# Kernel tuning notes

Hardware: AMD Instinct MI355X
Metric: run time of the kernel (lower is better)

Reference implementation:

```python
import jax, jax.numpy as jnp
import numpy as np

B, L, F, P, E, H, D, C, V = 256, 100, 8, 4, 64, 4, 64, 32, 10000
HD = H * D  # 256 = att_dim * head_num
TOWER_IN = F * E + F * E + P * E + C  # 1312
LN_EPS = 1e-3  # keras LayerNormalization default epsilon


def _ln(x, g, b):
    m = jnp.mean(x, axis=-1, keepdims=True)
    v = jnp.mean(jnp.square(x - m), axis=-1, keepdims=True)
    return (x - m) * jax.lax.rsqrt(v + LN_EPS) * g + b


def setup_inputs() -> dict:
    key = jax.random.key(0)
    ks = jax.random.split(key, 32)
    w = lambda k, s: jax.random.normal(k, s, jnp.float32) * 0.02
    inp = {
        'target_ad': jax.random.randint(ks[0], (B, F), 0, V),
        'ubs_feature': jax.random.randint(ks[1], (B, L, F), 0, V),
        'profile_feature': jax.random.randint(ks[2], (B, P), 0, V),
        'context_feature': jax.random.normal(ks[3], (B, C), jnp.float32),
        # embedding tables: one per sparse feature, stacked
        'item_tables': w(ks[4], (F, V, E)),
        'profile_tables': w(ks[5], (P, V, E)),
        # per-timestep distinct attention weights, stacked over L
        'q_w': w(ks[6], (L, E, HD)),
        'k_w': w(ks[7], (L, E, HD)),
        'v_w': w(ks[8], (L, E, HD)),
        'lin_w': w(ks[9], (L, HD, E)),
        'lin_b': jnp.zeros((L, E), jnp.float32),
        # shared post-attention layernorm
        'ln_g': jnp.ones((E,), jnp.float32),
        'ln_b': jnp.zeros((E,), jnp.float32),
        # dense tower
        't_w1': w(ks[10], (TOWER_IN, 1024)), 't_b1': jnp.zeros((1024,), jnp.float32),
        't_g1': jnp.ones((1024,), jnp.float32), 't_bb1': jnp.zeros((1024,), jnp.float32),
        't_w2': w(ks[11], (1024, 512)), 't_b2': jnp.zeros((512,), jnp.float32),
        't_g2': jnp.ones((512,), jnp.float32), 't_bb2': jnp.zeros((512,), jnp.float32),
        't_w3': w(ks[12], (512, 256)), 't_b3': jnp.zeros((256,), jnp.float32),
        't_g3': jnp.ones((256,), jnp.float32), 't_bb3': jnp.zeros((256,), jnp.float32),
        't_w4': w(ks[13], (256, 1)), 't_b4': jnp.zeros((1,), jnp.float32),
    }
    return inp


def reference(target_ad, ubs_feature, profile_feature, context_feature,
              item_tables, profile_tables, q_w, k_w, v_w, lin_w, lin_b,
              ln_g, ln_b,
              t_w1, t_b1, t_g1, t_bb1,
              t_w2, t_b2, t_g2, t_bb2,
              t_w3, t_b3, t_g3, t_bb3,
              t_w4, t_b4):
    b = target_ad.shape[0]
    # embedding lookups (feature-wise tables)
    te = item_tables[jnp.arange(F)[None, :], target_ad]              # [B,F,E]
    ue = item_tables[jnp.arange(F)[None, None, :], ubs_feature]      # [B,L,F,E]
    pe = profile_tables[jnp.arange(P)[None, :], profile_feature]     # [B,P,E]

    # per-step distinct Q/K/V projections, batched over L via einsum
    q = jnp.einsum('blfe,leo->blfo', ue, q_w).reshape(b, L, F, H, D)
    k = jnp.einsum('blfe,leo->blfo', ue, k_w).reshape(b, L, F, H, D)
    v = jnp.einsum('blfe,leo->blfo', ue, v_w).reshape(b, L, F, H, D)
    scores = jnp.einsum('blfhd,blghd->blhfg', q, k) / jnp.sqrt(jnp.float32(D))
    attw = jax.nn.softmax(scores, axis=-1)                           # [B,L,H,F,F]
    att = jnp.einsum('blhfg,blghd->blfhd', attw, v).reshape(b, L, F, HD)
    att_out = jnp.einsum('blfo,loe->blfe', att, lin_w) + lin_b[None, :, None, :]
    # shared LayerNorm per step, summed over L (original accumulates into zeros_like)
    ubs_t = jnp.sum(_ln(att_out, ln_g, ln_b), axis=1)                # [B,F,E]
    ubs = jax.nn.relu(ubs_t / jnp.float32(L))

    total = jnp.concatenate([ubs.reshape(b, -1), te.reshape(b, -1),
                             pe.reshape(b, -1), context_feature], axis=-1)

    h = jax.nn.relu(_ln(total @ t_w1 + t_b1, t_g1, t_bb1))
    h = jax.nn.relu(_ln(h @ t_w2 + t_b2, t_g2, t_bb2))
    h = jax.nn.relu(_ln(h @ t_w3 + t_b3, t_g3, t_bb3))
    out = jax.nn.sigmoid(h @ t_w4 + t_b4)                            # [B,1]
    return out
```

## Files before the change

kernel.cpp:

```cpp
#include <hip/hip_runtime.h>
#include <hip/hip_bf16.h>

#define B_ 256
#define L_ 100
#define F_ 8
#define P_ 4
#define E_ 64
#define H_ 4
#define D_ 64
#define C_ 32
#define V_ 10000
#define TOWER_IN_ 1312
#define LN_EPS 0.001f
#define LCHMAX_ 5
#define NCH_ 24
#define ZK_ 40
#define ATTN_BLKS_ (NCH_ * 32)

typedef __attribute__((ext_vector_type(8))) short bf8v;
typedef __attribute__((ext_vector_type(8))) unsigned short us8;
typedef __attribute__((ext_vector_type(4))) float f4v;

__device__ __forceinline__ unsigned short f2bf(float x) {
    __hip_bfloat16 h = __float2bfloat16(x);
    return __builtin_bit_cast(unsigned short, h);
}

#define BARRIER() do { \
    asm volatile("s_waitcnt lgkmcnt(0)" ::: "memory"); \
    __builtin_amdgcn_s_barrier(); \
    asm volatile("" ::: "memory"); \
} while (0)

__global__ __launch_bounds__(256) void pre_kernel(
    const float* __restrict__ q_w, const float* __restrict__ k_w,
    const float* __restrict__ v_w, const float* __restrict__ lin_w,
    unsigned short* __restrict__ wsMT, unsigned short* __restrict__ wsWT,
    float* __restrict__ ubs_acc)
{
    __shared__ float sA[64][68];
    __shared__ float sB[64][68];
    const int t = threadIdx.x;
    const int bx = blockIdx.x;

    if (bx >= 400) {
        const int bi = bx - 400;
        float4 z = {0.f, 0.f, 0.f, 0.f};
        *(float4*)(ubs_acc + (size_t)bi * 1024 + t * 4) = z;
        return;
    }

    const int l = bx >> 2;
    const int h = bx & 3;
    const size_t obase = (size_t)(l * 4 + h) * 4096;
    const int te = t & 15, to = t >> 4;

    for (int i = 0; i < 16; ++i) {
        int idx = t + i * 256;
        int e = idx >> 6, d = idx & 63;
        sA[e][d] = q_w[(l * 64 + e) * 256 + h * 64 + d];
        sB[e][d] = k_w[(l * 64 + e) * 256 + h * 64 + d];
    }
    __syncthreads();
    {
        float acc[4][4];
        #pragma unroll
        for (int i = 0; i < 4; ++i)
            #pragma unroll
            for (int j = 0; j < 4; ++j) acc[i][j] = 0.f;
        for (int d0 = 0; d0 < 64; d0 += 4) {
            float4 a4[4], b4[4];
            #pragma unroll
            for (int i = 0; i < 4; ++i) a4[i] = *(const float4*)&sA[te + 16 * i][d0];
            #pragma unroll
            for (int j = 0; j < 4; ++j) b4[j] = *(const float4*)&sB[to + 16 * j][d0];
            #pragma unroll
            for (int i = 0; i < 4; ++i)
                #pragma unroll
                for (int j = 0; j < 4; ++j) {
                    acc[i][j] += a4[i].x * b4[j].x;
                    acc[i][j] += a4[i].y * b4[j].y;
                    acc[i][j] += a4[i].z * b4[j].z;
                    acc[i][j] += a4[i].w * b4[j].w;
                }
        }
        #pragma unroll
        for (int j = 0; j < 4; ++j)
            #pragma unroll
            for (int i = 0; i < 4; ++i)
                wsMT[obase + (to + 16 * j) * 64 + (te + 16 * i)] = f2bf(acc[i][j]);
    }
    __syncthreads();

    for (int i = 0; i < 16; ++i) {
        int idx = t + i * 256;
        int e = idx >> 6, d = idx & 63;
        sA[e][d] = v_w[(l * 64 + e) * 256 + h * 64 + d];
        int oo = idx & 63, dd = idx >> 6;
        sB[oo][dd] = lin_w[l * 16384 + (h * 64 + dd) * 64 + oo];
    }
    __syncthreads();
    {
        float acc[4][4];
        #pragma unroll
        for (int i = 0; i < 4; ++i)
            #pragma unroll
            for (int j = 0; j < 4; ++j) acc[i][j] = 0.f;
        for (int d0 = 0; d0 < 64; d0 += 4) {
            float4 a4[4], b4[4];
            #pragma unroll
            for (int i = 0; i < 4; ++i) a4[i] = *(const float4*)&sA[te + 16 * i][d0];
            #pragma unroll
            for (int j = 0; j < 4; ++j) b4[j] = *(const float4*)&sB[to + 16 * j][d0];
            #pragma unroll
            for (int i = 0; i < 4; ++i)
                #pragma unroll
                for (int j = 0; j < 4; ++j) {
                    acc[i][j] += a4[i].x * b4[j].x;
                    acc[i][j] += a4[i].y * b4[j].y;
                    acc[i][j] += a4[i].z * b4[j].z;
                    acc[i][j] += a4[i].w * b4[j].w;
                }
        }
        #pragma unroll
        for (int j = 0; j < 4; ++j)
            #pragma unroll
            for (int i = 0; i < 4; ++i)
                wsWT[obase + (to + 16 * j) * 64 + (te + 16 * i)] = f2bf(acc[i][j]);
    }
}

__global__ __launch_bounds__(256, 3) void attn_kernel(
    const int* __restrict__ ubs_feature, const float* __restrict__ item_tables,
    const unsigned short* __restrict__ wsMT, const unsigned short* __restrict__ wsWT,
    const float* __restrict__ lin_b, const float* __restrict__ ln_g,
    const float* __restrict__ ln_b, float* __restrict__ ubs_acc,
    const float* __restrict__ w1, const float* __restrict__ w2,
    const float* __restrict__ w3,
    unsigned short* __restrict__ Wt1, unsigned short* __restrict__ Wt2,
    unsigned short* __restrict__ Wt3)
{
    __shared__ __align__(16) unsigned short sUE[64][72];
    __shared__ __align__(16) unsigned short sT[64][136];
    __shared__ __align__(16) unsigned short sZt[4][64][ZK_];
    __shared__ __align__(16) unsigned short sAblk[4][16][32];
    __shared__ float sLng[64], sLnb[64], sLinb[LCHMAX_][64];

    const int t = threadIdx.x;

    if (blockIdx.x >= ATTN_BLKS_) {
        float (*tile)[33] = (float (*)[33])sT;
        int bi = blockIdx.x - ATTN_BLKS_;
        const float* src; unsigned short* dst; int K, N, tk, tn;
        if (bi < 1312)      { src = w1; dst = Wt1; K = 1312; N = 1024; tk = bi / 32;  tn = bi % 32; }
        else if (bi < 1824) { int i = bi - 1312; src = w2; dst = Wt2; K = 1024; N = 512; tk = i / 16; tn = i % 16; }
        else                { int i = bi - 1824; src = w3; dst = Wt3; K = 512;  N = 256; tk = i / 8;  tn = i % 8; }
        const int k0 = tk * 32, n0 = tn * 32;
        const int rr = t >> 5, cc = t & 31;
        #pragma unroll
        for (int i = 0; i < 4; ++i) {
            int r = rr * 4 + i;
            tile[r][cc] = src[(size_t)(k0 + r) * N + n0 + cc];
        }
        __syncthreads();
        #pragma unroll
        for (int i = 0; i < 4; ++i) {
            int r = rr * 4 + i;
            dst[(size_t)(n0 + r) * K + k0 + cc] = f2bf(tile[cc][r]);
        }
        return;
    }

    const int c = blockIdx.x >> 5;
    const int lch   = (c < 4) ? 5 : 4;
    const int lbase = (c < 4) ? c * 5 : 20 + (c - 4) * 4;
    const int b0 = (blockIdx.x & 31) * 8;
    const int wv = t >> 6, lane = t & 63, quad = lane >> 4, cl = lane & 15;
    const int role = wv >> 1, hlw = wv & 1;

    const int grow = wv * 16 + (lane >> 2);
    const int gseg = lane & 3;
    const int gb = b0 + (grow >> 3), gf = grow & 7;

    if (t < 64) { sLng[t] = ln_g[t]; sLnb[t] = ln_b[t]; }
    if (t >= 64 && t < 128) {
        for (int li = 0; li < lch; ++li)
            sLinb[li][t - 64] = lin_b[(lbase + li) * 64 + (t - 64)];
    }

    int vidx[LCHMAX_];
    for (int li = 0; li < lch; ++li)
        vidx[li] = ubs_feature[(gb * L_ + lbase + li) * F_ + gf];

    float4 pf[4];
    bf8v bfrag[4][2];

    auto load_bfrag = [&](int lh) {
        const unsigned short* Bsrc = (role == 0 ? wsMT : wsWT) + ((size_t)lh * 4096);
        #pragma unroll
        for (int nt = 0; nt < 4; ++nt)
            #pragma unroll
            for (int k2 = 0; k2 < 2; ++k2)
                bfrag[nt][k2] = *(const bf8v*)(Bsrc + (nt * 16 + cl) * 64 + k2 * 32 + quad * 8);
    };
    auto load_pf = [&](int li) {
        const float* srcp = item_tables + ((size_t)gf * V_ + vidx[li]) * 64 + gseg * 16;
        #pragma unroll
        for (int j = 0; j < 4; ++j) pf[j] = ((const float4*)srcp)[j];
    };
    auto store_ue = [&]() {
        us8 u0, u1;
        u0[0] = f2bf(pf[0].x); u0[1] = f2bf(pf[0].y); u0[2] = f2bf(pf[0].z); u0[3] = f2bf(pf[0].w);
        u0[4] = f2bf(pf[1].x); u0[5] = f2bf(pf[1].y); u0[6] = f2bf(pf[1].z); u0[7] = f2bf(pf[1].w);
        u1[0] = f2bf(pf[2].x); u1[1] = f2bf(pf[2].y); u1[2] = f2bf(pf[2].z); u1[3] = f2bf(pf[2].w);
        u1[4] = f2bf(pf[3].x); u1[5] = f2bf(pf[3].y); u1[6] = f2bf(pf[3].z); u1[7] = f2bf(pf[3].w);
        *(us8*)&sUE[grow][gseg * 16]     = u0;
        *(us8*)&sUE[grow][gseg * 16 + 8] = u1;
    };

    load_pf(0);
    load_bfrag(lbase * 4 + hlw);
    store_ue();
    BARRIER();

    float lnacc[16];
    #pragma unroll
    for (int i = 0; i < 16; ++i) lnacc[i] = 0.f;

    for (int li = 0; li < lch; ++li) {
        const int l = lbase + li;

        if (li + 1 < lch) load_pf(li + 1);

        f4v accO[4];
        #pragma unroll
        for (int nt = 0; nt < 4; ++nt) accO[nt] = {0.f, 0.f, 0.f, 0.f};

        #pragma unroll
        for (int half = 0; half < 2; ++half) {
            #pragma unroll
            for (int m = 0; m < 4; ++m) {
                bf8v a0 = *(const bf8v*)&sUE[m * 16 + cl][quad * 8];
                bf8v a1 = *(const bf8v*)&sUE[m * 16 + cl][32 + quad * 8];
                #pragma unroll
                for (int nt = 0; nt < 4; ++nt) {
                    f4v acc = {0.f, 0.f, 0.f, 0.f};
                    acc = __builtin_amdgcn_mfma_f32_16x16x32_bf16(a0, bfrag[nt][0], acc, 0, 0, 0);
                    acc = __builtin_amdgcn_mfma_f32_16x16x32_bf16(a1, bfrag[nt][1], acc, 0, 0, 0);
                    if (role == 0) {
                        #pragma unroll
                        for (int j = 0; j < 4; ++j)
                            sT[m * 16 + quad * 4 + j][hlw * 64 + nt * 16 + cl] = f2bf(acc[j]);
                    } else {
                        ushort4 zp;
                        zp.x = f2bf(acc[0]); zp.y = f2bf(acc[1]);
                        zp.z = f2bf(acc[2]); zp.w = f2bf(acc[3]);
                        const int k0 = (quad >> 1) * 16 + hlw * 8 + (quad & 1) * 4;
                        *(ushort4*)&sZt[m][nt * 16 + cl][k0] = zp;
                    }
                }
            }
            if (half == 0)          load_bfrag(l * 4 + 2 + hlw);
            else if (li + 1 < lch)  load_bfrag((l + 1) * 4 + hlw);
            BARRIER();

            {
                const int p = wv;
                const bool valid = (cl >> 3) == (quad >> 1);
                bf8v u0 = *(const bf8v*)&sUE[p * 16 + cl][quad * 8];
                bf8v u1 = *(const bf8v*)&sUE[p * 16 + cl][32 + quad * 8];
                #pragma unroll
                for (int hl = 0; hl < 2; ++hl) {
                    bf8v a0s = *(const bf8v*)&sT[p * 16 + cl][hl * 64 + quad * 8];
                    bf8v a1s = *(const bf8v*)&sT[p * 16 + cl][hl * 64 + 32 + quad * 8];
                    f4v acc = {0.f, 0.f, 0.f, 0.f};
                    acc = __builtin_amdgcn_mfma_f32_16x16x32_bf16(a0s, u0, acc, 0, 0, 0);
                    acc = __builtin_amdgcn_mfma_f32_16x16x32_bf16(a1s, u1, acc, 0, 0, 0);
                    const int kk = hl * 8 + (cl & 7) + (cl >> 3) * 16;
                    #pragma unroll
                    for (int j = 0; j < 4; ++j) {
                        float v = acc[j] * 0.125f;
                        float mx = v;
                        mx = fmaxf(mx, __shfl_xor(mx, 1));
                        mx = fmaxf(mx, __shfl_xor(mx, 2));
                        mx = fmaxf(mx, __shfl_xor(mx, 4));
                        float ex = __expf(v - mx);
                        float sm = ex;
                        sm += __shfl_xor(sm, 1);
                        sm += __shfl_xor(sm, 2);
                        sm += __shfl_xor(sm, 4);
                        float aw = valid ? ex * __builtin_amdgcn_rcpf(sm) : 0.f;
                        sAblk[p][quad * 4 + j][kk] = f2bf(aw);
                    }
                }
            }

            {
                const int p = wv;
                bf8v a0p = *(const bf8v*)&sAblk[p][cl][quad * 8];
                #pragma unroll
                for (int nt = 0; nt < 4; ++nt) {
                    bf8v bz = *(const bf8v*)&sZt[p][nt * 16 + cl][quad * 8];
                    accO[nt] = __builtin_amdgcn_mfma_f32_16x16x32_bf16(a0p, bz, accO[nt], 0, 0, 0);
                }
            }
            if (half == 1 && li + 1 < lch) store_ue();
            BARRIER();
        }

        {
            float x[16];
            #pragma unroll
            for (int nt = 0; nt < 4; ++nt)
                #pragma unroll
                for (int j = 0; j < 4; ++j)
                    x[nt * 4 + j] = accO[nt][j] + sLinb[li][nt * 16 + cl];
            #pragma unroll
            for (int j = 0; j < 4; ++j) {
                float s = x[j] + x[4 + j] + x[8 + j] + x[12 + j];
                #pragma unroll
                for (int m = 1; m < 16; m <<= 1) s += __shfl_xor(s, m);
                float mean = s * (1.f / 64.f);
                float q = 0.f;
                #pragma unroll
                for (int nt = 0; nt < 4; ++nt) { float d = x[nt * 4 + j] - mean; q += d * d; }
                #pragma unroll
                for (int m = 1; m < 16; m <<= 1) q += __shfl_xor(q, m);
                float rst = rsqrtf(q * (1.f / 64.f) + LN_EPS);
                #pragma unroll
                for (int nt = 0; nt < 4; ++nt) {
                    int col = nt * 16 + cl;
                    lnacc[nt * 4 + j] += (x[nt * 4 + j] - mean) * rst * sLng[col] + sLnb[col];
                }
            }
        }
    }

    #pragma unroll
    for (int j = 0; j < 4; ++j) {
        const int row = wv * 16 + quad * 4 + j;
        const int b = b0 + (row >> 3), f = row & 7;
        #pragma unroll
        for (int nt = 0; nt < 4; ++nt)
            atomicAdd(&ubs_acc[(size_t)b * 512 + f * 64 + nt * 16 + cl], lnacc[nt * 4 + j]);
    }
}

__device__ __forceinline__ void gemm_from_lds(
    const unsigned short* sA, int lda,
    const unsigned short* __restrict__ Bw, const float* __restrict__ bias,
    float* __restrict__ Cd, int K, int N, int n0w, int m0,
    int quad, int cl)
{
    f4v acc0 = {0.f, 0.f, 0.f, 0.f};
    f4v acc1 = {0.f, 0.f, 0.f, 0.f};
    const unsigned short* arow = sA + cl * lda + quad * 8;
    const unsigned short* brow = Bw + (size_t)(n0w + cl) * K + quad * 8;
    int k0 = 0;
    for (; k0 + 64 <= K; k0 += 64) {
        bf8v a0 = *(const bf8v*)(arow + k0);
        bf8v b0 = *(const bf8v*)(brow + k0);
        bf8v a1 = *(const bf8v*)(arow + k0 + 32);
        bf8v b1 = *(const bf8v*)(brow + k0 + 32);
        acc0 = __builtin_amdgcn_mfma_f32_16x16x32_bf16(a0, b0, acc0, 0, 0, 0);
        acc1 = __builtin_amdgcn_mfma_f32_16x16x32_bf16(a1, b1, acc1, 0, 0, 0);
    }
    if (k0 < K) {
        bf8v a = *(const bf8v*)(arow + k0);
        bf8v b = *(const bf8v*)(brow + k0);
        acc0 = __builtin_amdgcn_mfma_f32_16x16x32_bf16(a, b, acc0, 0, 0, 0);
    }
    float bv = bias[n0w + cl];
    #pragma unroll
    for (int j = 0; j < 4; ++j)
        Cd[(size_t)(m0 + quad * 4 + j) * N + n0w + cl] = acc0[j] + acc1[j] + bv;
}

__device__ __forceinline__ void ln_rows_to_lds(
    const float* __restrict__ Cd, int N, int m0,
    const float* __restrict__ g, const float* __restrict__ bb,
    unsigned short* sH, int lda, int t, float invN)
{
    const int r = t >> 4, sub = t & 15;
    const float* crow = Cd + (size_t)(m0 + r) * N;
    float s = 0.f, s2 = 0.f;
    for (int j = sub * 4; j < N; j += 64) {
        float4 x = *(const float4*)(crow + j);
        s  += x.x + x.y + x.z + x.w;
        s2 += x.x * x.x + x.y * x.y + x.z * x.z + x.w * x.w;
    }
    #pragma unroll
    for (int m = 1; m < 16; m <<= 1) { s += __shfl_xor(s, m); s2 += __shfl_xor(s2, m); }
    const float mean = s * invN;
    const float var  = s2 * invN - mean * mean;
    const float rst  = rsqrtf(fmaxf(var, 0.f) + LN_EPS);
    for (int j = sub * 4; j < N; j += 64) {
        float4 x = *(const float4*)(crow + j);
        ushort4 o;
        o.x = f2bf(fmaxf((x.x - mean) * rst * g[j]     + bb[j],     0.f));
        o.y = f2bf(fmaxf((x.y - mean) * rst * g[j + 1] + bb[j + 1], 0.f));
        o.z = f2bf(fmaxf((x.z - mean) * rst * g[j + 2] + bb[j + 2], 0.f));
        o.w = f2bf(fmaxf((x.w - mean) * rst * g[j + 3] + bb[j + 3], 0.f));
        *(ushort4*)&sH[r * lda + j] = o;
    }
}

#define XLD 1320
__global__ __launch_bounds__(256) void gemm1x_kernel(
    const float* __restrict__ ubs_acc,
    const int* __restrict__ target_ad, const int* __restrict__ profile_feature,
    const float* __restrict__ context,
    const float* __restrict__ item_tables, const float* __restrict__ profile_tables,
    const unsigned short* __restrict__ Wt1, const float* __restrict__ b1,
    float* __restrict__ C1)
{
    __shared__ __align__(16) unsigned short sX[16][XLD];
    const int t = threadIdx.x;
    const int wv = t >> 6, lane = t & 63, quad = lane >> 4, cl = lane & 15;
    const int m0 = (blockIdx.x >> 4) * 16;
    const int n0w = (blockIdx.x & 15) * 64 + wv * 16;

    {
        const int r = t >> 4, sub = t & 15;
        const int gb = m0 + r;
        #pragma unroll
        for (int k = 0; k < 21; ++k) {
            int cc = sub * 4 + k * 64;
            if (cc >= TOWER_IN_) break;
            float4 x;
            if (cc < 512) {
                x = *(const float4*)(ubs_acc + (size_t)gb * 512 + cc);
                x.x = fmaxf(x.x * 0.01f, 0.f); x.y = fmaxf(x.y * 0.01f, 0.f);
                x.z = fmaxf(x.z * 0.01f, 0.f); x.w = fmaxf(x.w * 0.01f, 0.f);
            } else if (cc < 1024) {
                int f = (cc - 512) >> 6, e = (cc - 512) & 63;
                x = *(const float4*)(item_tables + ((size_t)f * V_ + target_ad[gb * 8 + f]) * 64 + e);
            } else if (cc < 1280) {
                int pp = (cc - 1024) >> 6, e = (cc - 1024) & 63;
                x = *(const float4*)(profile_tables + ((size_t)pp * V_ + profile_feature[gb * 4 + pp]) * 64 + e);
            } else {
                x = *(const float4*)(context + (size_t)gb * 32 + (cc - 1280));
            }
            ushort4 o;
            o.x = f2bf(x.x); o.y = f2bf(x.y); o.z = f2bf(x.z); o.w = f2bf(x.w);
            *(ushort4*)&sX[r][cc] = o;
        }
    }
    __syncthreads();
    gemm_from_lds(&sX[0][0], XLD, Wt1, b1, C1, 1312, 1024, n0w, m0, quad, cl);
}

#define H1LD 1032
__global__ __launch_bounds__(256) void gemm2f_kernel(
    const float* __restrict__ C1, const float* __restrict__ g1,
    const float* __restrict__ bb1,
    const unsigned short* __restrict__ Wt2, const float* __restrict__ b2,
    float* __restrict__ C2)
{
    __shared__ __align__(16) unsigned short sH[16][H1LD];
    const int t = threadIdx.x;
    const int wv = t >> 6, lane = t & 63, quad = lane >> 4, cl = lane & 15;
    const int m0 = (blockIdx.x >> 3) * 16;
    const int n0w = (blockIdx.x & 7) * 64 + wv * 16;

    ln_rows_to_lds(C1, 1024, m0, g1, bb1, &sH[0][0], H1LD, t, 1.f / 1024.f);
    __syncthreads();
    gemm_from_lds(&sH[0][0], H1LD, Wt2, b2, C2, 1024, 512, n0w, m0, quad, cl);
}

#define H2LD 520
__global__ __launch_bounds__(256) void gemm3f_kernel(
    const float* __restrict__ C2, const float* __restrict__ g2,
    const float* __restrict__ bb2,
    const unsigned short* __restrict__ Wt3, const float* __restrict__ b3,
    const float* __restrict__ g3, const float* __restrict__ bb3,
    const float* __restrict__ w4, const float* __restrict__ b4,
    float* __restrict__ out)
{
    __shared__ __align__(16) unsigned short sH[16][H2LD];
    __shared__ float sS[4][16], sQ[4][16], sP[4][16];
    const int t = threadIdx.x;
    const int wv = t >> 6, lane = t & 63, quad = lane >> 4, cl = lane & 15;
    const int m0 = blockIdx.x * 16;

    ln_rows_to_lds(C2, 512, m0, g2, bb2, &sH[0][0], H2LD, t, 1.f / 512.f);
    __syncthreads();

    f4v acc[4];
    #pragma unroll
    for (int nt = 0; nt < 4; ++nt) acc[nt] = {0.f, 0.f, 0.f, 0.f};
    for (int k0 = 0; k0 < 512; k0 += 32) {
        bf8v a = *(const bf8v*)&sH[cl][k0 + quad * 8];
        #pragma unroll
        for (int nt = 0; nt < 4; ++nt) {
            const int col0 = wv * 64 + nt * 16;
            bf8v b = *(const bf8v*)(Wt3 + (size_t)(col0 + cl) * 512 + k0 + quad * 8);
            acc[nt] = __builtin_amdgcn_mfma_f32_16x16x32_bf16(a, b, acc[nt], 0, 0, 0);
        }
    }
    #pragma unroll
    for (int nt = 0; nt < 4; ++nt) {
        float bv = b3[wv * 64 + nt * 16 + cl];
        #pragma unroll
        for (int j = 0; j < 4; ++j) acc[nt][j] += bv;
    }

    #pragma unroll
    for (int j = 0; j < 4; ++j) {
        float s = acc[0][j] + acc[1][j] + acc[2][j] + acc[3][j];
        float q = acc[0][j]*acc[0][j] + acc[1][j]*acc[1][j] + acc[2][j]*acc[2][j] + acc[3][j]*acc[3][j];
        #pragma unroll
        for (int m = 1; m < 16; m <<= 1) { s += __shfl_xor(s, m); q += __shfl_xor(q, m); }
        if (cl == 0) { sS[wv][quad * 4 + j] = s; sQ[wv][quad * 4 + j] = q; }
    }
    __syncthreads();
    float meanr[4], rstdr[4];
    #pragma unroll
    for (int j = 0; j < 4; ++j) {
        const int row = quad * 4 + j;
        float s = sS[0][row] + sS[1][row] + sS[2][row] + sS[3][row];
        float q = sQ[0][row] + sQ[1][row] + sQ[2][row] + sQ[3][row];
        float mean = s * (1.f / 256.f);
        float var  = q * (1.f / 256.f) - mean * mean;
        meanr[j] = mean;
        rstdr[j] = rsqrtf(fmaxf(var, 0.f) + LN_EPS);
    }

    #pragma unroll
    for (int j = 0; j < 4; ++j) {
        float p = 0.f;
        #pragma unroll
        for (int nt = 0; nt < 4; ++nt) {
            const int col = wv * 64 + nt * 16 + cl;
            float h = fmaxf((acc[nt][j] - meanr[j]) * rstdr[j] * g3[col] + bb3[col], 0.f);
            p += h * w4[col];
        }
        #pragma unroll
        for (int m = 1; m < 16; m <<= 1) p += __shfl_xor(p, m);
        if (cl == 0) sP[wv][quad * 4 + j] = p;
    }
    __syncthreads();
    if (t < 16) {
        float p = sP[0][t] + sP[1][t] + sP[2][t] + sP[3][t];
        out[m0 + t] = 1.f / (1.f + expf(-(p + b4[0])));
    }
}

extern "C" void kernel_launch(void* const* d_in, const int* in_sizes, int n_in,
                              void* d_out, int out_size, void* d_ws, size_t ws_size,
                              hipStream_t stream)
{
    (void)in_sizes; (void)n_in; (void)out_size; (void)ws_size;
    const int*   target_ad       = (const int*)d_in[0];
    const int*   ubs_feature     = (const int*)d_in[1];
    const int*   profile_feature = (const int*)d_in[2];
    const float* context         = (const float*)d_in[3];
    const float* item_tables     = (const float*)d_in[4];
    const float* profile_tables  = (const float*)d_in[5];
    const float* q_w   = (const float*)d_in[6];
    const float* k_w   = (const float*)d_in[7];
    const float* v_w   = (const float*)d_in[8];
    const float* lin_w = (const float*)d_in[9];
    const float* lin_b = (const float*)d_in[10];
    const float* ln_g  = (const float*)d_in[11];
    const float* ln_b  = (const float*)d_in[12];
    const float* t_w1  = (const float*)d_in[13];
    const float* t_b1  = (const float*)d_in[14];
    const float* t_g1  = (const float*)d_in[15];
    const float* t_bb1 = (const float*)d_in[16];
    const float* t_w2  = (const float*)d_in[17];
    const float* t_b2  = (const float*)d_in[18];
    const float* t_g2  = (const float*)d_in[19];
    const float* t_bb2 = (const float*)d_in[20];
    const float* t_w3  = (const float*)d_in[21];
    const float* t_b3  = (const float*)d_in[22];
    const float* t_g3  = (const float*)d_in[23];
    const float* t_bb3 = (const float*)d_in[24];
    const float* t_w4  = (const float*)d_in[25];
    const float* t_b4  = (const float*)d_in[26];

    char* ws = (char*)d_ws;
    unsigned short* wsMT = (unsigned short*)(ws);
    unsigned short* wsWT = (unsigned short*)(ws +  3276800);
    float* ubs_acc       = (float*)         (ws +  6553600);
    unsigned short* Wt1  = (unsigned short*)(ws +  7077888);
    unsigned short* Wt2  = (unsigned short*)(ws +  9764864);
    unsigned short* Wt3  = (unsigned short*)(ws + 10813440);
    float*          C1   = (float*)         (ws + 11075584);
    float*          C2   = (float*)         (ws + 12124160);

    pre_kernel<<<528, 256, 0, stream>>>(q_w, k_w, v_w, lin_w, wsMT, wsWT, ubs_acc);
    attn_kernel<<<ATTN_BLKS_ + 1952, 256, 0, stream>>>(ubs_feature, item_tables, wsMT, wsWT,
                                                       lin_b, ln_g, ln_b, ubs_acc,
                                                       t_w1, t_w2, t_w3, Wt1, Wt2, Wt3);
    gemm1x_kernel<<<256, 256, 0, stream>>>(ubs_acc, target_ad, profile_feature, context,
                                           item_tables, profile_tables, Wt1, t_b1, C1);
    gemm2f_kernel<<<128, 256, 0, stream>>>(C1, t_g1, t_bb1, Wt2, t_b2, C2);
    gemm3f_kernel<<<16, 256, 0, stream>>>(C2, t_g2, t_bb2, Wt3, t_b3,
                                          t_g3, t_bb3, t_w4, t_b4, (float*)d_out);
}
```

Measured before the change: 242.3 us.

## Split K across two wave groups in tower GEMMs and raise MFMA wave priority

The first two dense-tower GEMM kernels now launch 512 threads per block. Two groups of four waves each compute half of the K range, and the partial sums are combined through shared memory before the store. The row-staging and LayerNorm loaders are widened to use all 512 threads. The attention kernel also wraps its MFMA sections in s_setprio so those waves get issue priority. The intent is more parallelism and shorter per-wave dependency chains in small-grid GEMMs, at the cost of an extra barrier, an LDS reduction, and fewer resident blocks per CU.

```diff
diff --git a/kernel.cpp b/kernel.cpp
--- a/kernel.cpp
+++ b/kernel.cpp
@@ -238,6 +238,7 @@
 
         #pragma unroll
         for (int half = 0; half < 2; ++half) {
+            __builtin_amdgcn_s_setprio(1);
             #pragma unroll
             for (int m = 0; m < 4; ++m) {
                 bf8v a0 = *(const bf8v*)&sUE[m * 16 + cl][quad * 8];
@@ -260,6 +261,7 @@
                     }
                 }
             }
+            __builtin_amdgcn_s_setprio(0);
             if (half == 0)          load_bfrag(l * 4 + 2 + hlw);
             else if (li + 1 < lch)  load_bfrag((l + 1) * 4 + hlw);
             BARRIER();
@@ -298,11 +300,13 @@
             {
                 const int p = wv;
                 bf8v a0p = *(const bf8v*)&sAblk[p][cl][quad * 8];
+                __builtin_amdgcn_s_setprio(1);
                 #pragma unroll
                 for (int nt = 0; nt < 4; ++nt) {
                     bf8v bz = *(const bf8v*)&sZt[p][nt * 16 + cl][quad * 8];
                     accO[nt] = __builtin_amdgcn_mfma_f32_16x16x32_bf16(a0p, bz, accO[nt], 0, 0, 0);
                 }
+                __builtin_amdgcn_s_setprio(0);
             }
             if (half == 1 && li + 1 < lch) store_ue();
             BARRIER();
@@ -346,55 +350,50 @@
     }
 }
 
-__device__ __forceinline__ void gemm_from_lds(
-    const unsigned short* sA, int lda,
-    const unsigned short* __restrict__ Bw, const float* __restrict__ bias,
-    float* __restrict__ Cd, int K, int N, int n0w, int m0,
-    int quad, int cl)
+__device__ __forceinline__ f4v gemm_krange(
+    const unsigned short* sArow, const unsigned short* __restrict__ brow,
+    int klo, int khi)
 {
     f4v acc0 = {0.f, 0.f, 0.f, 0.f};
     f4v acc1 = {0.f, 0.f, 0.f, 0.f};
-    const unsigned short* arow = sA + cl * lda + quad * 8;
-    const unsigned short* brow = Bw + (size_t)(n0w + cl) * K + quad * 8;
-    int k0 = 0;
-    for (; k0 + 64 <= K; k0 += 64) {
-        bf8v a0 = *(const bf8v*)(arow + k0);
+    int k0 = klo;
+    for (; k0 + 64 <= khi; k0 += 64) {
+        bf8v a0 = *(const bf8v*)(sArow + k0);
         bf8v b0 = *(const bf8v*)(brow + k0);
-        bf8v a1 = *(const bf8v*)(arow + k0 + 32);
+        bf8v a1 = *(const bf8v*)(sArow + k0 + 32);
         bf8v b1 = *(const bf8v*)(brow + k0 + 32);
         acc0 = __builtin_amdgcn_mfma_f32_16x16x32_bf16(a0, b0, acc0, 0, 0, 0);
         acc1 = __builtin_amdgcn_mfma_f32_16x16x32_bf16(a1, b1, acc1, 0, 0, 0);
     }
-    if (k0 < K) {
-        bf8v a = *(const bf8v*)(arow + k0);
+    if (k0 < khi) {
+        bf8v a = *(const bf8v*)(sArow + k0);
         bf8v b = *(const bf8v*)(brow + k0);
         acc0 = __builtin_amdgcn_mfma_f32_16x16x32_bf16(a, b, acc0, 0, 0, 0);
     }
-    float bv = bias[n0w + cl];
-    #pragma unroll
-    for (int j = 0; j < 4; ++j)
-        Cd[(size_t)(m0 + quad * 4 + j) * N + n0w + cl] = acc0[j] + acc1[j] + bv;
-}
-
-__device__ __forceinline__ void ln_rows_to_lds(
+    #pragma unroll
+    for (int j = 0; j < 4; ++j) acc0[j] += acc1[j];
+    return acc0;
+}
+
+__device__ __forceinline__ void ln_rows_to_lds512(
     const float* __restrict__ Cd, int N, int m0,
     const float* __restrict__ g, const float* __restrict__ bb,
     unsigned short* sH, int lda, int t, float invN)
 {
-    const int r = t >> 4, sub = t & 15;
+    const int r = t >> 5, sub = t & 31;
     const float* crow = Cd + (size_t)(m0 + r) * N;
     float s = 0.f, s2 = 0.f;
-    for (int j = sub * 4; j < N; j += 64) {
+    for (int j = sub * 4; j < N; j += 128) {
         float4 x = *(const float4*)(crow + j);
         s  += x.x + x.y + x.z + x.w;
         s2 += x.x * x.x + x.y * x.y + x.z * x.z + x.w * x.w;
     }
     #pragma unroll
-    for (int m = 1; m < 16; m <<= 1) { s += __shfl_xor(s, m); s2 += __shfl_xor(s2, m); }
+    for (int m = 1; m < 32; m <<= 1) { s += __shfl_xor(s, m); s2 += __shfl_xor(s2, m); }
     const float mean = s * invN;
     const float var  = s2 * invN - mean * mean;
     const float rst  = rsqrtf(fmaxf(var, 0.f) + LN_EPS);
-    for (int j = sub * 4; j < N; j += 64) {
+    for (int j = sub * 4; j < N; j += 128) {
         float4 x = *(const float4*)(crow + j);
         ushort4 o;
         o.x = f2bf(fmaxf((x.x - mean) * rst * g[j]     + bb[j],     0.f));
@@ -406,7 +405,7 @@
 }
 
 #define XLD 1320
-__global__ __launch_bounds__(256) void gemm1x_kernel(
+__global__ __launch_bounds__(512) void gemm1x_kernel(
     const float* __restrict__ ubs_acc,
     const int* __restrict__ target_ad, const int* __restrict__ profile_feature,
     const float* __restrict__ context,
@@ -415,17 +414,19 @@
     float* __restrict__ C1)
 {
     __shared__ __align__(16) unsigned short sX[16][XLD];
+    __shared__ float sRed[4][16][16];
     const int t = threadIdx.x;
     const int wv = t >> 6, lane = t & 63, quad = lane >> 4, cl = lane & 15;
+    const int nw = wv & 3, kh = wv >> 2;
     const int m0 = (blockIdx.x >> 4) * 16;
-    const int n0w = (blockIdx.x & 15) * 64 + wv * 16;
+    const int n0w = (blockIdx.x & 15) * 64 + nw * 16;
 
     {
-        const int r = t >> 4, sub = t & 15;
+        const int r = t >> 5, sub = t & 31;
         const int gb = m0 + r;
         #pragma unroll
-        for (int k = 0; k < 21; ++k) {
-            int cc = sub * 4 + k * 64;
+        for (int k = 0; k < 11; ++k) {
+            int cc = sub * 4 + k * 128;
             if (cc >= TOWER_IN_) break;
             float4 x;
             if (cc < 512) {
@@ -447,25 +448,88 @@
         }
     }
     __syncthreads();
-    gemm_from_lds(&sX[0][0], XLD, Wt1, b1, C1, 1312, 1024, n0w, m0, quad, cl);
+
+    const unsigned short* arow = &sX[0][0] + cl * XLD + quad * 8;
+    const unsigned short* brow = Wt1 + (size_t)(n0w + cl) * 1312 + quad * 8;
+    f4v part = gemm_krange(arow, brow, kh ? 672 : 0, kh ? 1312 : 672);
+
+    if (kh == 1) {
+        #pragma unroll
+        for (int j = 0; j < 4; ++j) sRed[nw][quad * 4 + j][cl] = part[j];
+    }
+    __syncthreads();
+    if (kh == 0) {
+        float bv = b1[n0w + cl];
+        #pragma unroll
+        for (int j = 0; j < 4; ++j)
+            C1[(size_t)(m0 + quad * 4 + j) * 1024 + n0w + cl] =
+                part[j] + sRed[nw][quad * 4 + j][cl] + bv;
+    }
 }
 
 #define H1LD 1032
-__global__ __launch_bounds__(256) void gemm2f_kernel(
+__global__ __launch_bounds__(512) void gemm2f_kernel(
     const float* __restrict__ C1, const float* __restrict__ g1,
     const float* __restrict__ bb1,
     const unsigned short* __restrict__ Wt2, const float* __restrict__ b2,
     float* __restrict__ C2)
 {
     __shared__ __align__(16) unsigned short sH[16][H1LD];
+    __shared__ float sRed[4][16][16];
     const int t = threadIdx.x;
     const int wv = t >> 6, lane = t & 63, quad = lane >> 4, cl = lane & 15;
+    const int nw = wv & 3, kh = wv >> 2;
     const int m0 = (blockIdx.x >> 3) * 16;
-    const int n0w = (blockIdx.x & 7) * 64 + wv * 16;
-
-    ln_rows_to_lds(C1, 1024, m0, g1, bb1, &sH[0][0], H1LD, t, 1.f / 1024.f);
-    __syncthreads();
-    gemm_from_lds(&sH[0][0], H1LD, Wt2, b2, C2, 1024, 512, n0w, m0, quad, cl);
+    const int n0w = (blockIdx.x & 7) * 64 + nw * 16;
+
+    ln_rows_to_lds512(C1, 1024, m0, g1, bb1, &sH[0][0], H1LD, t, 1.f / 1024.f);
+    __syncthreads();
+
+    const unsigned short* arow = &sH[0][0] + cl * H1LD + quad * 8;
+    const unsigned short* brow = Wt2 + (size_t)(n0w + cl) * 1024 + quad * 8;
+    f4v part = gemm_krange(arow, brow, kh ? 512 : 0, kh ? 1024 : 512);
+
+    if (kh == 1) {
+        #pragma unroll
+        for (int j = 0; j < 4; ++j) sRed[nw][quad * 4 + j][cl] = part[j];
+    }
+    __syncthreads();
+    if (kh == 0) {
+        float bv = b2[n0w + cl];
+        #pragma unroll
+        for (int j = 0; j < 4; ++j)
+            C2[(size_t)(m0 + quad * 4 + j) * 512 + n0w + cl] =
+                part[j] + sRed[nw][quad * 4 + j][cl] + bv;
+    }
+}
+
+__device__ __forceinline__ void ln_rows_to_lds(
+    const float* __restrict__ Cd, int N, int m0,
+    const float* __restrict__ g, const float* __restrict__ bb,
+    unsigned short* sH, int lda, int t, float invN)
+{
+    const int r = t >> 4, sub = t & 15;
+    const float* crow = Cd + (size_t)(m0 + r) * N;
+    float s = 0.f, s2 = 0.f;
+    for (int j = sub * 4; j < N; j += 64) {
+        float4 x = *(const float4*)(crow + j);
+        s  += x.x + x.y + x.z + x.w;
+        s2 += x.x * x.x + x.y * x.y + x.z * x.z + x.w * x.w;
+    }
+    #pragma unroll
+    for (int m = 1; m < 16; m <<= 1) { s += __shfl_xor(s, m); s2 += __shfl_xor(s2, m); }
+    const float mean = s * invN;
+    const float var  = s2 * invN - mean * mean;
+    const float rst  = rsqrtf(fmaxf(var, 0.f) + LN_EPS);
+    for (int j = sub * 4; j < N; j += 64) {
+        float4 x = *(const float4*)(crow + j);
+        ushort4 o;
+        o.x = f2bf(fmaxf((x.x - mean) * rst * g[j]     + bb[j],     0.f));
+        o.y = f2bf(fmaxf((x.y - mean) * rst * g[j + 1] + bb[j + 1], 0.f));
+        o.z = f2bf(fmaxf((x.z - mean) * rst * g[j + 2] + bb[j + 2], 0.f));
+        o.w = f2bf(fmaxf((x.w - mean) * rst * g[j + 3] + bb[j + 3], 0.f));
+        *(ushort4*)&sH[r * lda + j] = o;
+    }
 }
 
 #define H2LD 520
@@ -593,9 +657,9 @@
     attn_kernel<<<ATTN_BLKS_ + 1952, 256, 0, stream>>>(ubs_feature, item_tables, wsMT, wsWT,
                                                        lin_b, ln_g, ln_b, ubs_acc,
                                                        t_w1, t_w2, t_w3, Wt1, Wt2, Wt3);
-    gemm1x_kernel<<<256, 256, 0, stream>>>(ubs_acc, target_ad, profile_feature, context,
+    gemm1x_kernel<<<256, 512, 0, stream>>>(ubs_acc, target_ad, profile_feature, context,
                                            item_tables, profile_tables, Wt1, t_b1, C1);
-    gemm2f_kernel<<<128, 256, 0, stream>>>(C1, t_g1, t_bb1, Wt2, t_b2, C2);
+    gemm2f_kernel<<<128, 512, 0, stream>>>(C1, t_g1, t_bb1, Wt2, t_b2, C2);
     gemm3f_kernel<<<16, 256, 0, stream>>>(C2, t_g2, t_bb2, Wt3, t_b3,
                                           t_g3, t_bb3, t_w4, t_b4, (float*)d_out);
 }
```

After: 233.8 us. -3.5%, faster.
